# Kernel optimization log

Hardware: AMD Instinct MI355X
Metric: run time of the kernel (lower is better)

The kernel has to match this reference:

```python
import math
import jax
import jax.numpy as jnp
import numpy as np

MUL = 32            # multiplicity of 0e and 1o in irreps_in/out
N_NODES = 50000
N_EDGES = 800000
N_BASIS = 10
N_HID = 100
NUM_NEIGHBORS = 16.0


def setup_inputs() -> dict:
    key = jax.random.key(0)
    ks = jax.random.split(key, 14)
    return {
        "node_input": jax.random.normal(ks[0], (N_NODES, 4 * MUL), jnp.float32),
        "node_attr": jnp.ones((N_NODES, 1), jnp.float32),
        "edge_src": jax.random.randint(ks[1], (N_EDGES,), 0, N_NODES, dtype=jnp.int32),
        "edge_dst": jax.random.randint(ks[2], (N_EDGES,), 0, N_NODES, dtype=jnp.int32),
        "edge_attr": jax.random.normal(ks[3], (N_EDGES, 4), jnp.float32),
        "edge_length_embedded": jax.random.uniform(ks[4], (N_EDGES, N_BASIS), dtype=jnp.float32),
        "W_sc0": jax.random.normal(ks[5], (MUL, MUL), jnp.float32),
        "W_sc1": jax.random.normal(ks[6], (MUL, MUL), jnp.float32),
        "W_l10": jax.random.normal(ks[7], (MUL, MUL), jnp.float32),
        "W_l11": jax.random.normal(ks[8], (MUL, MUL), jnp.float32),
        "W_l20": jax.random.normal(ks[9], (2 * MUL, MUL), jnp.float32),
        "W_l21": jax.random.normal(ks[10], (2 * MUL, MUL), jnp.float32),
        "W_fc1": jax.random.normal(ks[11], (N_BASIS, N_HID), jnp.float32),
        "W_fc2": jax.random.normal(ks[12], (N_HID, 4 * MUL), jnp.float32),
    }


def _fctp(x0, x1, attr, W0, W1):
    """FullyConnectedTensorProduct with a 1x0e attr: per-irrep linear * scalar attr.
    x0: [N,U], x1: [N,U,3], attr: [N,1]. Path norm alpha = 1/sqrt(fan_in)."""
    inv = 1.0 / math.sqrt(W0.shape[0])
    o0 = attr * (x0 @ W0) * inv                                    # [N,W]
    o1 = attr[:, :, None] * jnp.einsum("nud,uw->nwd", x1, W1) * inv  # [N,W,3]
    return o0, o1


def _forward(node_input, node_attr, edge_attr, edge_length_embedded,
             W_sc0, W_sc1, W_l10, W_l11, W_l20, W_l21, W_fc1, W_fc2,
             edge_src, edge_dst):
    N = node_input.shape[0]
    x0 = node_input[:, :MUL]                       # [N,32]  0e
    x1 = node_input[:, MUL:].reshape(N, MUL, 3)    # [N,32,3] 1o

    # self-connection and lin1 (both attr is scalar 0e)
    s0, s1 = _fctp(x0, x1, node_attr, W_sc0, W_sc1)
    y0, y1 = _fctp(x0, x1, node_attr, W_l10, W_l11)

    # radial MLP -> per-edge uvu weights (weight_numel = 4*MUL)
    h = jax.nn.silu(edge_length_embedded @ W_fc1 * (1.0 / math.sqrt(N_BASIS)))
    w = h @ W_fc2 * (1.0 / math.sqrt(N_HID))       # [E,128]
    w1, w2, w3, w4 = (w[:, 0*MUL:1*MUL], w[:, 1*MUL:2*MUL],
                      w[:, 2*MUL:3*MUL], w[:, 3*MUL:4*MUL])

    # gather source node features per edge
    x0s = y0[edge_src]                              # [E,32]
    x1s = y1[edge_src]                              # [E,32,3]
    ea0 = edge_attr[:, :1]                          # [E,1]   0e
    ea1 = edge_attr[:, 1:]                          # [E,3]   1o

    # segmented uvu tensor product (CG for lmax=1, component norm)
    mid0a = w1 * x0s * ea0                                         # 0e x 0e -> 0e
    mid0b = w4 * jnp.einsum("eum,em->eu", x1s, ea1) * (1.0 / math.sqrt(3.0))  # 1o x 1o -> 0e
    mid1a = (w2 * x0s)[:, :, None] * ea1[:, None, :]               # 0e x 1o -> 1o
    mid1b = w3[:, :, None] * x1s * ea0[:, None, :]                 # 1o x 0e -> 1o
    E = edge_attr.shape[0]
    edge_features = jnp.concatenate(
        [mid0a, mid0b, mid1a.reshape(E, -1), mid1b.reshape(E, -1)], axis=1)  # [E,256]

    # scatter-add to destination nodes
    agg = jax.ops.segment_sum(edge_features, edge_dst, num_segments=N)
    agg = agg * (1.0 / math.sqrt(NUM_NEIGHBORS))

    m0 = agg[:, :2 * MUL]                           # [N,64]  0e part of irreps_mid
    m1 = agg[:, 2 * MUL:].reshape(N, 2 * MUL, 3)    # [N,64,3] 1o part
    z0, z1 = _fctp(m0, m1, node_attr, W_l20, W_l21)

    # sc output_mask is all ones (every output irrep reachable)
    c_s = math.sin(math.pi / 8.0)
    c_x = math.cos(math.pi / 8.0)
    out0 = c_s * s0 + c_x * z0
    out1 = c_s * s1 + c_x * z1
    return jnp.concatenate([out0, out1.reshape(N, -1)], axis=1)   # [N,128]


def reference(node_input, node_attr, edge_src, edge_dst, edge_attr, edge_length_embedded,
              W_sc0, W_sc1, W_l10, W_l11, W_l20, W_l21, W_fc1, W_fc2):
    return _forward(node_input, node_attr, edge_attr, edge_length_embedded,
                    W_sc0, W_sc1, W_l10, W_l11, W_l20, W_l21, W_fc1, W_fc2,
                    edge_src, edge_dst)
```

## Files before the change

kernel.cpp:

```cpp
#include <hip/hip_runtime.h>
#include <hip/hip_bf16.h>

#define MUL 32
#define F4 128
#define NB 10
#define NH 100
#define EROW 136
#define REC 48

#define INV_SQRT32 0.17677669529663687f
#define INV_SQRT10 0.31622776601683794f
#define INV_SQRT100 0.1f
#define INV_SQRT3 0.5773502691896258f
#define AGG_SCALE 0.25f
#define INV8 0.125f
#define C_S 0.3826834323650898f
#define C_X 0.9238795325112867f

typedef __attribute__((ext_vector_type(8))) short short8;
typedef __attribute__((ext_vector_type(4))) float float4v;

__device__ __forceinline__ float bf2f(__hip_bfloat16 v) { return __bfloat162float(v); }
__device__ __forceinline__ unsigned short f2b(float x) {
    __hip_bfloat16 b = __float2bfloat16(x);
    return *(unsigned short*)&b;
}
__device__ __forceinline__ float b2f(unsigned short u) {
    __hip_bfloat16 b;
    *(unsigned short*)&b = u;
    return __bfloat162float(b);
}
__device__ __forceinline__ float ldin(const void* p, size_t i, int f) {
    return f ? ((const float*)p)[i] : bf2f(((const __hip_bfloat16*)p)[i]);
}

__global__ void detect_dtype_kernel(const void* __restrict__ node_attr, int* __restrict__ flag) {
    unsigned w = *(const unsigned*)node_attr;
    *flag = (w == 0x3F800000u) ? 1 : 0;
}

__global__ __launch_bounds__(256) void prep_kernel(
    const void* __restrict__ Wfc1,
    const void* __restrict__ Wfc2,
    const void* __restrict__ Wl20,
    const void* __restrict__ Wl21,
    const int* __restrict__ flagp,
    unsigned short* __restrict__ w1t,
    unsigned short* __restrict__ w2t,
    unsigned short* __restrict__ w20t,
    unsigned short* __restrict__ w21t)
{
    int f = *flagp;
    int gi = blockIdx.x * 256 + threadIdx.x;
    if (gi < 128 * 128) {
        int n = gi >> 7, k = gi & 127;
        w2t[gi] = (k < NH) ? f2b(ldin(Wfc2, (size_t)k * 128 + n, f)) : 0;
    }
    if (gi < 32 * 64) {
        int v = gi >> 6, u = gi & 63;
        w20t[gi] = f2b(ldin(Wl20, (size_t)u * 32 + v, f));
        w21t[gi] = f2b(ldin(Wl21, (size_t)u * 32 + v, f));
    }
    if (gi < 112 * 32) {
        int n = gi >> 5, k = gi & 31;
        w1t[gi] = (k < NB && n < NH) ? f2b(ldin(Wfc1, (size_t)k * NH + n, f)) : 0;
    }
}

__global__ __launch_bounds__(256) void hist_kernel(
    const int* __restrict__ edst, int* __restrict__ cnt, int E)
{
    int i = blockIdx.x * 256 + threadIdx.x;
    if (i < E) atomicAdd(&cnt[edst[i]], 1);
}

__global__ __launch_bounds__(1024) void scanA_kernel(
    int* __restrict__ cnt, int* __restrict__ bsum, int N)
{
    __shared__ int wsum[16];
    int t = threadIdx.x, lane = t & 63, wid = t >> 6;
    int i = blockIdx.x * 1024 + t;
    int v = (i < N) ? cnt[i] : 0;
    int x = v;
#pragma unroll
    for (int d = 1; d < 64; d <<= 1) { int yv = __shfl_up(x, d); if (lane >= d) x += yv; }
    if (lane == 63) wsum[wid] = x;
    __syncthreads();
    if (wid == 0 && lane < 16) {
        int s = wsum[lane];
#pragma unroll
        for (int d = 1; d < 16; d <<= 1) { int yv = __shfl_up(s, d); if (lane >= d) s += yv; }
        wsum[lane] = s;
    }
    __syncthreads();
    int pre = (wid > 0 ? wsum[wid - 1] : 0);
    if (i < N) cnt[i] = pre + x - v;
    if (t == 0) bsum[blockIdx.x] = wsum[15];
}

__global__ __launch_bounds__(64) void scanB_kernel(int* __restrict__ bsum, int nb)
{
    int t = threadIdx.x;
    int carry = 0;
    for (int c0 = 0; c0 < nb; c0 += 64) {
        int idx = c0 + t;
        int v = (idx < nb) ? bsum[idx] : 0;
        int x = v;
#pragma unroll
        for (int d = 1; d < 64; d <<= 1) { int yv = __shfl_up(x, d); if (t >= d) x += yv; }
        if (idx < nb) bsum[idx] = carry + x - v;
        carry += __shfl(x, 63);
    }
}

__global__ __launch_bounds__(1024) void scanC_kernel(
    int* __restrict__ cnt, const int* __restrict__ bsum, int N)
{
    int i = blockIdx.x * 1024 + threadIdx.x;
    if (i < N) cnt[i] += bsum[blockIdx.x];
}

__global__ __launch_bounds__(256) void scatter_build_kernel(
    const int* __restrict__ edst,
    const int* __restrict__ esrc,
    const void* __restrict__ eattr,
    const void* __restrict__ ele,
    const int* __restrict__ flagp,
    int* __restrict__ cnt,
    unsigned char* __restrict__ rec, int E)
{
    int i = blockIdx.x * 256 + threadIdx.x;
    if (i >= E) return;
    int f = *flagp;
    int d = edst[i];
    int p = atomicAdd(&cnt[d], 1);

    unsigned e0 = f2b(ldin(ele, (size_t)i * NB + 0, f));
    unsigned e1 = f2b(ldin(ele, (size_t)i * NB + 1, f));
    unsigned e2 = f2b(ldin(ele, (size_t)i * NB + 2, f));
    unsigned e3 = f2b(ldin(ele, (size_t)i * NB + 3, f));
    unsigned e4 = f2b(ldin(ele, (size_t)i * NB + 4, f));
    unsigned e5 = f2b(ldin(ele, (size_t)i * NB + 5, f));
    unsigned e6 = f2b(ldin(ele, (size_t)i * NB + 6, f));
    unsigned e7 = f2b(ldin(ele, (size_t)i * NB + 7, f));
    unsigned e8 = f2b(ldin(ele, (size_t)i * NB + 8, f));
    unsigned e9 = f2b(ldin(ele, (size_t)i * NB + 9, f));
    float ea0 = ldin(eattr, (size_t)i * 4 + 0, f);
    float ea1 = ldin(eattr, (size_t)i * 4 + 1, f);
    float ea2 = ldin(eattr, (size_t)i * 4 + 2, f);
    float ea3 = ldin(eattr, (size_t)i * 4 + 3, f);

    unsigned char* r = rec + (size_t)p * REC;
    *(int4*)(r + 0)  = make_int4(esrc[i], d, (int)(e0 | (e1 << 16)), (int)(e2 | (e3 << 16)));
    *(int4*)(r + 16) = make_int4((int)(e4 | (e5 << 16)), (int)(e6 | (e7 << 16)), (int)(e8 | (e9 << 16)), 0);
    *(float4*)(r + 32) = make_float4(ea0, ea1, ea2, ea3);
}

__global__ __launch_bounds__(256) void node_y_kernel(
    const void* __restrict__ node_input,
    const void* __restrict__ node_attr,
    const void* __restrict__ Wl10,
    const void* __restrict__ Wl11,
    const int* __restrict__ flagp,
    unsigned short* __restrict__ y, int N)
{
    __shared__ float sW0[1024];
    __shared__ float sW1[1024];
    __shared__ float sX[16 * 128];
    int f = *flagp;
    int t = threadIdx.x;
    for (int i = t; i < 1024; i += 256) {
        sW0[i] = ldin(Wl10, i, f);
        sW1[i] = ldin(Wl11, i, f);
    }
    int n0 = blockIdx.x * 16;
    for (int i = t; i < 2048; i += 256) {
        int ln = i >> 7, c = i & 127, n = n0 + ln;
        sX[i] = (n < N) ? ldin(node_input, (size_t)n * F4 + c, f) : 0.f;
    }
    __syncthreads();
    for (int i = t; i < 2048; i += 256) {
        int ln = i >> 7, c = i & 127, n = n0 + ln;
        if (n >= N) continue;
        float attr = ldin(node_attr, n, f);
        float acc = 0.f;
        if (c < 32) {
#pragma unroll
            for (int u = 0; u < 32; u++) acc += sX[ln * 128 + u] * sW0[u * 32 + c];
        } else {
            int d = (c - 32) >> 5, u0 = (c - 32) & 31;
#pragma unroll
            for (int u = 0; u < 32; u++) acc += sX[ln * 128 + 32 + u * 3 + d] * sW1[u * 32 + u0];
        }
        y[(size_t)n * F4 + c] = f2b(acc * attr * INV_SQRT32);
    }
}

#define SM_ELEB  0
#define SM_HW    4096
#define SM_EA    21504
#define SM_SRC   22528
#define SM_DST   22784
#define SM_TOTAL 23040

__global__ __launch_bounds__(256, 6) void fused_edge_kernel(
    const unsigned char* __restrict__ rec,
    const int* __restrict__ cnt,
    const unsigned short* __restrict__ y,
    const unsigned short* __restrict__ w1t,
    const unsigned short* __restrict__ w2t,
    const unsigned short* __restrict__ w20t,
    const unsigned short* __restrict__ w21t,
    float* __restrict__ agg,
    int E)
{
    __shared__ __align__(16) char smem[SM_TOTAL];
    unsigned short* sEleB = (unsigned short*)(smem + SM_ELEB);
    unsigned short* sHW = (unsigned short*)(smem + SM_HW);
    float* sEa = (float*)(smem + SM_EA);
    int* sSrc = (int*)(smem + SM_SRC);
    int* sDst = (int*)(smem + SM_DST);

    int t = threadIdx.x;
    int base = blockIdx.x * 64;
    int ne = E - base;
    if (ne > 64) ne = 64;

    if (t < 64) {
        if (t < ne) {
            int2 sd = *(const int2*)(rec + (size_t)(base + t) * REC);
            sSrc[t] = sd.x;
            sDst[t] = sd.y;
        } else {
            sSrc[t] = 0;
            sDst[t] = -1;
        }
    }
    for (int i = t; i < 64 * 32; i += 256) {
        int e = i >> 5, k = i & 31;
        unsigned short v = 0;
        if (k < NB && e < ne)
            v = *(const unsigned short*)(rec + (size_t)(base + e) * REC + 8 + 2 * k);
        sEleB[i] = v;
    }
    {
        int e = t >> 2;
        sEa[t] = (e < ne) ? *(const float*)(rec + (size_t)(base + e) * REC + 32 + 4 * (t & 3)) : 0.f;
    }
    __syncthreads();

    int w = t >> 6, lane = t & 63;
    int lm = lane & 15, quad = lane >> 4;
    int em = w * 16 + lm;

    const unsigned short* yrg = y + (size_t)sSrc[em] * 128;
    short8 x0  = *(const short8*)(yrg + quad * 8);
    short8 xd0 = *(const short8*)(yrg + 32 + quad * 8);
    short8 xd1 = *(const short8*)(yrg + 64 + quad * 8);
    short8 xd2 = *(const short8*)(yrg + 96 + quad * 8);

    {
        short8 a = *(const short8*)(sEleB + (w * 16 + lm) * 32 + quad * 8);
        float4v c1[7];
#pragma unroll
        for (int nt = 0; nt < 7; nt++) {
            c1[nt] = (float4v){0.f, 0.f, 0.f, 0.f};
            short8 b = *(const short8*)(w1t + (nt * 16 + lm) * 32 + quad * 8);
            c1[nt] = __builtin_amdgcn_mfma_f32_16x16x32_bf16(a, b, c1[nt], 0, 0, 0);
        }
#pragma unroll
        for (int nt = 0; nt < 7; nt++) {
            int ch = nt * 16 + lm;
#pragma unroll
            for (int r = 0; r < 4; r++) {
                int row = w * 16 + quad * 4 + r;
                float hv = 0.f;
                if (ch < NH) {
                    float aa = c1[nt][r] * INV_SQRT10;
                    hv = aa / (1.f + __expf(-aa));
                }
                sHW[row * EROW + ch] = f2b(hv);
            }
        }
        int e = t >> 2, seg = t & 3;
        *(uint2*)(sHW + e * EROW + 112 + seg * 4) = (uint2){0u, 0u};
    }
    __syncthreads();

    short8 hfr[4];
#pragma unroll
    for (int kc = 0; kc < 4; kc++)
        hfr[kc] = *(const short8*)(sHW + (w * 16 + lm) * EROW + kc * 32 + quad * 8);
    __syncthreads();
    {
        float4v c2[8];
#pragma unroll
        for (int nt = 0; nt < 8; nt++) c2[nt] = (float4v){0.f, 0.f, 0.f, 0.f};
#pragma unroll
        for (int kc = 0; kc < 4; kc++) {
#pragma unroll
            for (int nt = 0; nt < 8; nt++) {
                short8 b = *(const short8*)(w2t + (nt * 16 + lm) * 128 + kc * 32 + quad * 8);
                c2[nt] = __builtin_amdgcn_mfma_f32_16x16x32_bf16(hfr[kc], b, c2[nt], 0, 0, 0);
            }
        }
#pragma unroll
        for (int nt = 0; nt < 8; nt++)
#pragma unroll
            for (int r = 0; r < 4; r++)
                sHW[(w * 16 + quad * 4 + r) * EROW + nt * 16 + lm] = f2b(c2[nt][r] * INV_SQRT100);
    }
    __syncthreads();

    {
        const unsigned short* wr = sHW + em * EROW;
        short8 wA = *(const short8*)(wr + quad * 8);
        short8 wB = *(const short8*)(wr + 32 + quad * 8);
        short8 wC = *(const short8*)(wr + 64 + quad * 8);
        short8 wD = *(const short8*)(wr + 96 + quad * 8);
        float ea0 = sEa[em * 4 + 0];
        float e1x = sEa[em * 4 + 1];
        float e1y = sEa[em * 4 + 2];
        float e1z = sEa[em * 4 + 3];
        float ea0S = ea0 * AGG_SCALE;
        float s3 = AGG_SCALE * INV_SQRT3;

        short8 f00, f01, f10, f11, f20, f21, f30, f31;
#pragma unroll
        for (int j = 0; j < 8; j++) {
            float x0f = b2f((unsigned short)x0[j]);
            float d0f = b2f((unsigned short)xd0[j]);
            float d1f = b2f((unsigned short)xd1[j]);
            float d2f = b2f((unsigned short)xd2[j]);
            f00[j] = (short)f2b(b2f((unsigned short)wA[j]) * x0f * ea0S);
            float tt = d0f * e1x + d1f * e1y + d2f * e1z;
            f01[j] = (short)f2b(b2f((unsigned short)wD[j]) * tt * s3);
            float p = b2f((unsigned short)wB[j]) * x0f * AGG_SCALE;
            f10[j] = (short)f2b(p * e1x);
            f20[j] = (short)f2b(p * e1y);
            f30[j] = (short)f2b(p * e1z);
            float q = b2f((unsigned short)wC[j]) * ea0S;
            f11[j] = (short)f2b(q * d0f);
            f21[j] = (short)f2b(q * d1f);
            f31[j] = (short)f2b(q * d2f);
        }

        float4v acc[8];
#pragma unroll
        for (int i = 0; i < 8; i++) acc[i] = (float4v){0.f, 0.f, 0.f, 0.f};
#pragma unroll
        for (int g = 0; g < 4; g++) {
            const unsigned short* wt = g ? w21t : w20t;
            short8 ak0 = (g == 0) ? f00 : (g == 1) ? f10 : (g == 2) ? f20 : f30;
            short8 ak1 = (g == 0) ? f01 : (g == 1) ? f11 : (g == 2) ? f21 : f31;
#pragma unroll
            for (int nt = 0; nt < 2; nt++) {
                short8 b0 = *(const short8*)(wt + (nt * 16 + lm) * 64 + quad * 8);
                short8 b1 = *(const short8*)(wt + (nt * 16 + lm) * 64 + 32 + quad * 8);
                acc[g * 2 + nt] = __builtin_amdgcn_mfma_f32_16x16x32_bf16(ak0, b0, acc[g * 2 + nt], 0, 0, 0);
                acc[g * 2 + nt] = __builtin_amdgcn_mfma_f32_16x16x32_bf16(ak1, b1, acc[g * 2 + nt], 0, 0, 0);
            }
        }

        __syncthreads();
        unsigned short* sFeat = (unsigned short*)smem;
#pragma unroll
        for (int g = 0; g < 4; g++)
#pragma unroll
            for (int nt = 0; nt < 2; nt++) {
                int ch = (g == 0) ? (nt * 16 + lm) : (32 + (g - 1) * 32 + nt * 16 + lm);
#pragma unroll
                for (int r = 0; r < 4; r++) {
                    int er = w * 16 + quad * 4 + r;
                    sFeat[er * EROW + ch] = f2b(acc[g * 2 + nt][r]);
                }
            }
        __syncthreads();

        if (t < 128) {
            int c = t;
            int e = 0;
            while (e < ne) {
                int d = sDst[e];
                int rs = e;
                do { e++; } while (e < ne && sDst[e] == d);
                if (d < 0) continue;
                float s = 0.f;
                for (int q = rs; q < e; q++) s += b2f(sFeat[q * EROW + c]);
                int bs = (d > 0) ? cnt[d - 1] : 0;
                int be = cnt[d];
                if (bs >= base && be <= base + ne)
                    agg[(size_t)d * F4 + c] = s;
                else
                    atomicAdd(&agg[(size_t)d * F4 + c], s);
            }
        }
    }
}

__global__ __launch_bounds__(256) void out_kernel(
    const void* __restrict__ node_input,
    const void* __restrict__ node_attr,
    const void* __restrict__ Wsc0,
    const void* __restrict__ Wsc1,
    const float* __restrict__ agg,
    const int* __restrict__ flagp,
    void* __restrict__ out, int N)
{
    __shared__ float sWs0[1024], sWs1[1024];
    __shared__ float sX[16 * 128];
    __shared__ float sA[16 * 128];
    int f = *flagp;
    int t = threadIdx.x;
    for (int i = t; i < 1024; i += 256) {
        sWs0[i] = ldin(Wsc0, i, f);
        sWs1[i] = ldin(Wsc1, i, f);
    }
    int n0 = blockIdx.x * 16;
    for (int i = t; i < 2048; i += 256) {
        int ln = i >> 7, c = i & 127, n = n0 + ln;
        sX[i] = (n < N) ? ldin(node_input, (size_t)n * F4 + c, f) : 0.f;
        sA[i] = (n < N) ? agg[(size_t)n * F4 + c] : 0.f;
    }
    __syncthreads();
    for (int i = t; i < 2048; i += 256) {
        int ln = i >> 7, c = i & 127, n = n0 + ln;
        if (n >= N) continue;
        float attr = ldin(node_attr, n, f);
        float s, z;
        if (c < 32) {
            float as = 0.f;
#pragma unroll
            for (int u = 0; u < 32; u++) as += sX[ln * 128 + u] * sWs0[u * 32 + c];
            s = as * INV_SQRT32;
            z = sA[ln * 128 + c];
        } else {
            int i2 = c - 32;
            int u0 = i2 / 3, d = i2 - u0 * 3;
            float as = 0.f;
#pragma unroll
            for (int u = 0; u < 32; u++) as += sX[ln * 128 + 32 + u * 3 + d] * sWs1[u * 32 + u0];
            s = as * INV_SQRT32;
            z = sA[ln * 128 + 32 + d * 32 + u0];
        }
        float val = attr * (C_S * s + C_X * z * INV8);
        size_t oi = (size_t)n * F4 + c;
        if (f) ((float*)out)[oi] = val;
        else   ((__hip_bfloat16*)out)[oi] = __float2bfloat16(val);
    }
}

extern "C" void kernel_launch(void* const* d_in, const int* in_sizes, int n_in,
                              void* d_out, int out_size, void* d_ws, size_t ws_size,
                              hipStream_t stream) {
    const void* node_input = d_in[0];
    const void* node_attr  = d_in[1];
    const int* edge_src    = (const int*)d_in[2];
    const int* edge_dst    = (const int*)d_in[3];
    const void* edge_attr  = d_in[4];
    const void* ele        = d_in[5];
    const void* Wsc0       = d_in[6];
    const void* Wsc1       = d_in[7];
    const void* Wl10       = d_in[8];
    const void* Wl11       = d_in[9];
    const void* Wl20       = d_in[10];
    const void* Wl21       = d_in[11];
    const void* Wfc1       = d_in[12];
    const void* Wfc2       = d_in[13];

    int N = in_sizes[0] / F4;
    int E = in_sizes[2];

    char* ws = (char*)d_ws;
    int* flag = (int*)ws;
    unsigned short* y = (unsigned short*)(ws + 64);
    size_t y_b = (size_t)N * F4 * 2;
    float* agg = (float*)(ws + 64 + y_b);
    size_t agg_b = (size_t)N * F4 * 4;
    size_t off = 64 + y_b + agg_b;
    unsigned short* w2t  = (unsigned short*)(ws + off);
    unsigned short* w20t = (unsigned short*)(ws + off + 32768);
    unsigned short* w21t = (unsigned short*)(ws + off + 36864);
    unsigned short* w1t  = (unsigned short*)(ws + off + 40960);
    size_t off2 = off + 49152;
    int* cnt = (int*)(ws + off2);
    size_t cnt_b = ((size_t)N * 4 + 63) & ~(size_t)63;
    int* bsum = (int*)(ws + off2 + cnt_b);
    size_t bsum_b = 4096;
    unsigned char* rec = (unsigned char*)(ws + off2 + cnt_b + bsum_b);

    int nscan = (N + 1023) / 1024;

    detect_dtype_kernel<<<1, 1, 0, stream>>>(node_attr, flag);
    prep_kernel<<<64, 256, 0, stream>>>(Wfc1, Wfc2, Wl20, Wl21, flag, w1t, w2t, w20t, w21t);
    (void)hipMemsetAsync(cnt, 0, (size_t)N * 4, stream);
    (void)hipMemsetAsync(agg, 0, agg_b, stream);

    hist_kernel<<<(E + 255) / 256, 256, 0, stream>>>(edge_dst, cnt, E);
    scanA_kernel<<<nscan, 1024, 0, stream>>>(cnt, bsum, N);
    scanB_kernel<<<1, 64, 0, stream>>>(bsum, nscan);
    scanC_kernel<<<nscan, 1024, 0, stream>>>(cnt, bsum, N);
    scatter_build_kernel<<<(E + 255) / 256, 256, 0, stream>>>(
        edge_dst, edge_src, edge_attr, ele, flag, cnt, rec, E);

    node_y_kernel<<<(N + 15) / 16, 256, 0, stream>>>(node_input, node_attr, Wl10, Wl11, flag, y, N);

    fused_edge_kernel<<<(E + 63) / 64, 256, 0, stream>>>(
        rec, cnt, y, w1t, w2t, w20t, w21t, agg, E);

    out_kernel<<<(N + 15) / 16, 256, 0, stream>>>(node_input, node_attr, Wsc0, Wsc1,
                                                  agg, flag, d_out, N);
}
```

Before: 673.5 us.

## Interleave MFMA tiles with epilogue stores and relax launch bounds to four waves

Restructures the three MFMA stages so each output tile is computed and immediately written to shared memory, rather than first accumulating all tiles in register arrays and storing them afterwards. This lowers the number of accumulator registers live at once. At the same time the launch bound minimum is lowered from 6 to 4 blocks per CU, which lets the compiler use more registers. The catch is that the MFMA latency of each tile is now serialized against its dependent stores, with fewer independent MFMAs available to hide it.

Result: faster. 642.4 us (-4.6%).

```diff
diff --git a/kernel.cpp b/kernel.cpp
--- a/kernel.cpp
+++ b/kernel.cpp
@@ -203,7 +203,7 @@
 #define SM_DST   22784
 #define SM_TOTAL 23040
 
-__global__ __launch_bounds__(256, 6) void fused_edge_kernel(
+__global__ __launch_bounds__(256, 4) void fused_edge_kernel(
     const unsigned char* __restrict__ rec,
     const int* __restrict__ cnt,
     const unsigned short* __restrict__ y,
@@ -261,22 +261,18 @@
 
     {
         short8 a = *(const short8*)(sEleB + (w * 16 + lm) * 32 + quad * 8);
-        float4v c1[7];
 #pragma unroll
         for (int nt = 0; nt < 7; nt++) {
-            c1[nt] = (float4v){0.f, 0.f, 0.f, 0.f};
+            float4v c1 = (float4v){0.f, 0.f, 0.f, 0.f};
             short8 b = *(const short8*)(w1t + (nt * 16 + lm) * 32 + quad * 8);
-            c1[nt] = __builtin_amdgcn_mfma_f32_16x16x32_bf16(a, b, c1[nt], 0, 0, 0);
-        }
-#pragma unroll
-        for (int nt = 0; nt < 7; nt++) {
+            c1 = __builtin_amdgcn_mfma_f32_16x16x32_bf16(a, b, c1, 0, 0, 0);
             int ch = nt * 16 + lm;
 #pragma unroll
             for (int r = 0; r < 4; r++) {
                 int row = w * 16 + quad * 4 + r;
                 float hv = 0.f;
                 if (ch < NH) {
-                    float aa = c1[nt][r] * INV_SQRT10;
+                    float aa = c1[r] * INV_SQRT10;
                     hv = aa / (1.f + __expf(-aa));
                 }
                 sHW[row * EROW + ch] = f2b(hv);
@@ -292,23 +288,17 @@
     for (int kc = 0; kc < 4; kc++)
         hfr[kc] = *(const short8*)(sHW + (w * 16 + lm) * EROW + kc * 32 + quad * 8);
     __syncthreads();
-    {
-        float4v c2[8];
-#pragma unroll
-        for (int nt = 0; nt < 8; nt++) c2[nt] = (float4v){0.f, 0.f, 0.f, 0.f};
+#pragma unroll
+    for (int nt = 0; nt < 8; nt++) {
+        float4v c2 = (float4v){0.f, 0.f, 0.f, 0.f};
 #pragma unroll
         for (int kc = 0; kc < 4; kc++) {
-#pragma unroll
-            for (int nt = 0; nt < 8; nt++) {
-                short8 b = *(const short8*)(w2t + (nt * 16 + lm) * 128 + kc * 32 + quad * 8);
-                c2[nt] = __builtin_amdgcn_mfma_f32_16x16x32_bf16(hfr[kc], b, c2[nt], 0, 0, 0);
-            }
-        }
-#pragma unroll
-        for (int nt = 0; nt < 8; nt++)
-#pragma unroll
-            for (int r = 0; r < 4; r++)
-                sHW[(w * 16 + quad * 4 + r) * EROW + nt * 16 + lm] = f2b(c2[nt][r] * INV_SQRT100);
+            short8 b = *(const short8*)(w2t + (nt * 16 + lm) * 128 + kc * 32 + quad * 8);
+            c2 = __builtin_amdgcn_mfma_f32_16x16x32_bf16(hfr[kc], b, c2, 0, 0, 0);
+        }
+#pragma unroll
+        for (int r = 0; r < 4; r++)
+            sHW[(w * 16 + quad * 4 + r) * EROW + nt * 16 + lm] = f2b(c2[r] * INV_SQRT100);
     }
     __syncthreads();
 
@@ -345,9 +335,8 @@
             f31[j] = (short)f2b(q * d2f);
         }
 
-        float4v acc[8];
-#pragma unroll
-        for (int i = 0; i < 8; i++) acc[i] = (float4v){0.f, 0.f, 0.f, 0.f};
+        __syncthreads();
+        unsigned short* sFeat = (unsigned short*)smem;
 #pragma unroll
         for (int g = 0; g < 4; g++) {
             const unsigned short* wt = g ? w21t : w20t;
@@ -355,26 +344,19 @@
             short8 ak1 = (g == 0) ? f01 : (g == 1) ? f11 : (g == 2) ? f21 : f31;
 #pragma unroll
             for (int nt = 0; nt < 2; nt++) {
+                float4v acc = (float4v){0.f, 0.f, 0.f, 0.f};
                 short8 b0 = *(const short8*)(wt + (nt * 16 + lm) * 64 + quad * 8);
                 short8 b1 = *(const short8*)(wt + (nt * 16 + lm) * 64 + 32 + quad * 8);
-                acc[g * 2 + nt] = __builtin_amdgcn_mfma_f32_16x16x32_bf16(ak0, b0, acc[g * 2 + nt], 0, 0, 0);
-                acc[g * 2 + nt] = __builtin_amdgcn_mfma_f32_16x16x32_bf16(ak1, b1, acc[g * 2 + nt], 0, 0, 0);
-            }
-        }
-
-        __syncthreads();
-        unsigned short* sFeat = (unsigned short*)smem;
-#pragma unroll
-        for (int g = 0; g < 4; g++)
-#pragma unroll
-            for (int nt = 0; nt < 2; nt++) {
+                acc = __builtin_amdgcn_mfma_f32_16x16x32_bf16(ak0, b0, acc, 0, 0, 0);
+                acc = __builtin_amdgcn_mfma_f32_16x16x32_bf16(ak1, b1, acc, 0, 0, 0);
                 int ch = (g == 0) ? (nt * 16 + lm) : (32 + (g - 1) * 32 + nt * 16 + lm);
 #pragma unroll
                 for (int r = 0; r < 4; r++) {
                     int er = w * 16 + quad * 4 + r;
-                    sFeat[er * EROW + ch] = f2b(acc[g * 2 + nt][r]);
+                    sFeat[er * EROW + ch] = f2b(acc[r]);
                 }
             }
+        }
         __syncthreads();
 
         if (t < 128) {
```
